# Kernel optimization log

Measured on AMD Instinct MI355X. Metric: run time of the kernel, lower is better.

The kernel has to match this reference:

```python
import jax, jax.numpy as jnp
import numpy as np

B, S, D, H = 2, 2048, 1024, 16
HD = D // H  # head_dim = 64


def setup_inputs() -> dict:
    key = jax.random.key(0)
    k1, k2, k3 = jax.random.split(key, 3)
    x = jax.random.normal(k1, (B, S, D), dtype=jnp.float32)
    mask = jnp.zeros((B, S, S), dtype=jnp.float32)  # additive mask
    # Dense(3*D) params (glorot-ish scale) and Dense(D) output projection
    Wqkv = jax.random.normal(k2, (D, 3 * D), dtype=jnp.float32) * (1.0 / np.sqrt(D))
    bqkv = jnp.zeros((3 * D,), dtype=jnp.float32)
    Wo = jax.random.normal(k3, (D, D), dtype=jnp.float32) * (1.0 / np.sqrt(D))
    bo = jnp.zeros((D,), dtype=jnp.float32)
    return {"x": x, "mask": mask, "Wqkv": Wqkv, "bqkv": bqkv, "Wo": Wo, "bo": bo}


def reference(x, mask, Wqkv, bqkv, Wo, bo):
    b, s, d = x.shape
    qkv = x @ Wqkv + bqkv                              # [B,S,3D]
    qkv = qkv.reshape(b, s, H, 3 * HD).transpose(0, 2, 1, 3)  # [B,H,S,3*HD]
    q, k, v = jnp.split(qkv, 3, axis=-1)               # each [B,H,S,HD]
    scale = 1.0 / jnp.sqrt(jnp.float32(HD))
    scores = jnp.einsum('bhqd,bhkd->bhqk', q, k) * scale  # [B,H,S,S]
    scores = scores + mask[:, None, :, :]
    attn = jax.nn.softmax(scores, axis=-1)
    values = jnp.einsum('bhqk,bhkd->bhqd', attn, v)    # [B,H,S,HD]
    # Faithful to original: reshape WITHOUT transposing heads back
    values = values.reshape(b, s, H * HD)              # [B,S,D]
    return values @ Wo + bo
```

## Files before the change

### kernel.cpp

```cpp
#include <hip/hip_runtime.h>
#include <hip/hip_bf16.h>

#define B_ 2
#define S_ 2048
#define D_ 1024
#define H_ 16
#define HD_ 64

typedef __attribute__((ext_vector_type(8))) short short8;
typedef __attribute__((ext_vector_type(4))) float f32x4;
typedef __attribute__((ext_vector_type(16))) float f32x16;
typedef __attribute__((ext_vector_type(4))) unsigned short us4;

static __device__ __forceinline__ ushort f2bf(float x) {
  __hip_bfloat16 h = __float2bfloat16(x);
  return *reinterpret_cast<ushort*>(&h);
}

static __device__ __forceinline__ void gld_lds16(void* lds, const void* g) {
  __builtin_amdgcn_global_load_lds(
      (__attribute__((address_space(1))) void*)(g),
      (__attribute__((address_space(3))) void*)(lds), 16, 0, 0);
}


static __device__ __forceinline__ void transpose_tile(const float* __restrict__ in,
                                                      ushort* __restrict__ out,
                                                      int K, int N, int bn, int bk,
                                                      int tx, int ty) {
  __shared__ float tile[32][33];
  #pragma unroll
  for (int i = ty; i < 32; i += 8)
    tile[i][tx] = in[(size_t)(bk + i) * N + bn + tx];
  __syncthreads();
  #pragma unroll
  for (int i = ty; i < 32; i += 8)
    out[(size_t)(bn + i) * K + bk + tx] = f2bf(tile[tx][i]);
}

__global__ __launch_bounds__(256) void prep_all(const float4* __restrict__ x4,
                                                ushort* __restrict__ xbf,
                                                const float* __restrict__ Wqkv,
                                                ushort* __restrict__ wqkvT,
                                                const float* __restrict__ Wo,
                                                ushort* __restrict__ woT) {
  const int blk = blockIdx.x, tid = threadIdx.x;
  if (blk < 4096) {
    const int i = blk * 256 + tid;
    float4 v = x4[i];
    ushort4 o;
    o.x = f2bf(v.x); o.y = f2bf(v.y); o.z = f2bf(v.z); o.w = f2bf(v.w);
    *reinterpret_cast<ushort4*>(xbf + (size_t)i * 4) = o;
  } else if (blk < 7168) {
    const int sub = blk - 4096;
    transpose_tile(Wqkv, wqkvT, D_, 3 * D_, (sub % 96) * 32, (sub / 96) * 32,
                   tid & 31, tid >> 5);
  } else {
    const int sub = blk - 7168;
    transpose_tile(Wo, woT, D_, D_, (sub % 32) * 32, (sub / 32) * 32,
                   tid & 31, tid >> 5);
  }
}

template <bool OUT_BF16>
__global__ __launch_bounds__(256) void gemm_bt(const ushort* __restrict__ A,
                                               const ushort* __restrict__ Bt,
                                               const float* __restrict__ bias,
                                               ushort* __restrict__ Cb,
                                               float* __restrict__ Cf,
                                               int M, int N, int K) {
  __shared__ __align__(16) ushort As[128 * 32];
  __shared__ __align__(16) ushort Bs[128 * 32];
  const int tid = threadIdx.x;
  const int lane = tid & 63, wid = tid >> 6;
  const int wr = wid >> 1, wc = wid & 1;

  const int nwg = gridDim.x * gridDim.y;
  const int lin = blockIdx.x + gridDim.x * blockIdx.y;
  const int nl = (lin & 7) * (nwg >> 3) + (lin >> 3);
  const int row0 = (nl % gridDim.x) * 128, col0 = (nl / gridDim.x) * 128;

  const int l15 = lane & 15, lhi = lane >> 4;

  f32x4 acc[4][4];
  #pragma unroll
  for (int i = 0; i < 4; ++i)
    #pragma unroll
    for (int j = 0; j < 4; ++j)
      acc[i][j] = f32x4{0.f, 0.f, 0.f, 0.f};

  const int sr = tid >> 2;
  const int scol = (tid & 3) * 8;

  for (int k0 = 0; k0 < K; k0 += 32) {
    gld_lds16(&As[(size_t)tid * 8],        &A[(size_t)(row0 + sr) * K + k0 + scol]);
    gld_lds16(&As[2048 + (size_t)tid * 8], &A[(size_t)(row0 + 64 + sr) * K + k0 + scol]);
    gld_lds16(&Bs[(size_t)tid * 8],        &Bt[(size_t)(col0 + sr) * K + k0 + scol]);
    gld_lds16(&Bs[2048 + (size_t)tid * 8], &Bt[(size_t)(col0 + 64 + sr) * K + k0 + scol]);
    __syncthreads();

    short8 af[4], bfr[4];
    #pragma unroll
    for (int mt = 0; mt < 4; ++mt)
      af[mt] = *(const short8*)&As[(wr * 64 + mt * 16 + l15) * 32 + lhi * 8];
    #pragma unroll
    for (int nt = 0; nt < 4; ++nt)
      bfr[nt] = *(const short8*)&Bs[(wc * 64 + nt * 16 + l15) * 32 + lhi * 8];
    #pragma unroll
    for (int mt = 0; mt < 4; ++mt)
      #pragma unroll
      for (int nt = 0; nt < 4; ++nt)
        acc[mt][nt] = __builtin_amdgcn_mfma_f32_16x16x32_bf16(af[mt], bfr[nt], acc[mt][nt], 0, 0, 0);
    __syncthreads();
  }

  const int orow = row0 + wr * 64;
  const int ocol = col0 + wc * 64 + l15;
  #pragma unroll
  for (int mt = 0; mt < 4; ++mt) {
    #pragma unroll
    for (int nt = 0; nt < 4; ++nt) {
      const int gc = ocol + nt * 16;
      const float bv = bias[gc];
      #pragma unroll
      for (int r = 0; r < 4; ++r) {
        const int gr = orow + mt * 16 + lhi * 4 + r;
        const float v = acc[mt][nt][r] + bv;
        if (OUT_BF16) Cb[(size_t)gr * N + gc] = f2bf(v);
        else          Cf[(size_t)gr * N + gc] = v;
      }
    }
  }
}

__global__ __launch_bounds__(256, 2) void flash_attn(const ushort* __restrict__ qkv,
                                                     const float* __restrict__ mask,
                                                     ushort* __restrict__ values) {
  __shared__ __align__(16) ushort Ks[2][64 * 64];
  __shared__ __align__(16) ushort Vt[2][64 * 64];

  const int tid = threadIdx.x;
  const int lane = tid & 63, wid = tid >> 6;
  const int l31 = lane & 31, lhalf = lane >> 5;
  const int qt = blockIdx.x, bh = blockIdx.y, b = bh >> 4, h = bh & 15;
  const size_t base = (size_t)b * S_ * 3072 + (size_t)h * 192;
  const int q = qt * 128 + wid * 32 + l31;
  const int NT = S_ / 64;

  short8 qf[4];
  {
    const ushort* qrow = qkv + base + (size_t)q * 3072 + lhalf * 8;
    qf[0] = *(const short8*)(qrow);
    qf[1] = *(const short8*)(qrow + 16);
    qf[2] = *(const short8*)(qrow + 32);
    qf[3] = *(const short8*)(qrow + 48);
  }

  const int srow = tid >> 3, sch = tid & 7;
  const int hsr = (srow ^ (srow >> 3)) & 7;
  const int scs = sch ^ hsr;
  const int kg = tid & 15, d0 = (tid >> 4) * 4;
  const int skg = (kg & 12) | ((kg & 1) << 1) | ((kg >> 1) & 1);

  float m_run = -3.0e38f, l_run = 0.f;
  f32x16 o[2];
  #pragma unroll
  for (int dg = 0; dg < 2; ++dg)
    #pragma unroll
    for (int i = 0; i < 16; ++i) o[dg][i] = 0.f;

  const float* mrow = mask + ((size_t)b * S_ + q) * S_;
  us4 vr[4];
  f32x16 scA[2], scB[2];

#define QKT_(SCDST, KSBUF)                                                     \
  {                                                                            \
    _Pragma("unroll")                                                          \
    for (int g = 0; g < 2; ++g) {                                              \
      const int row_ = g * 32 + l31;                                           \
      const int hk_ = (row_ ^ (row_ >> 3)) & 7;                                \
      const ushort* kp_ = &(KSBUF)[row_ * 64];                                 \
      f32x16 s_;                                                               \
      _Pragma("unroll")                                                        \
      for (int i = 0; i < 16; ++i) s_[i] = 0.f;                                \
      _Pragma("unroll")                                                        \
      for (int kd = 0; kd < 4; ++kd) {                                         \
        short8 kf_ = *(const short8*)&kp_[(((kd * 2 + lhalf) ^ hk_) & 7) * 8]; \
        s_ = __builtin_amdgcn_mfma_f32_32x32x16_bf16(kf_, qf[kd], s_, 0, 0, 0);\
      }                                                                        \
      (SCDST)[g] = s_;                                                         \
    }                                                                          \
  }

#define VSCATTER_(VTBUF)                                                       \
  {                                                                            \
    _Pragma("unroll")                                                          \
    for (int dd = 0; dd < 4; ++dd) {                                           \
      const int d_ = d0 + dd;                                                  \
      const int hd_ = (d_ ^ (d_ >> 3)) & 7;                                    \
      us4 w_;                                                                  \
      w_[0] = vr[0][dd]; w_[1] = vr[1][dd];                                    \
      w_[2] = vr[2][dd]; w_[3] = vr[3][dd];                                    \
      *(us4*)&(VTBUF)[d_ * 64 + (((skg >> 1) ^ hd_) & 7) * 8 + (skg & 1) * 4] = w_; \
    }                                                                          \
  }

#define HALF_(T, SCCUR, SCNEXT)                                                \
  {                                                                            \
    const int t_ = (T);                                                        \
    const bool pre1_ = (t_ + 1 < NT), pre2_ = (t_ + 2 < NT);                   \
    if (pre2_) {                                                               \
      const ushort* kn_ = qkv + base + (size_t)(t_ + 2) * 64 * 3072 +          \
                          (size_t)srow * 3072 + 64;                            \
      gld_lds16(&Ks[t_ & 1][tid * 8],        kn_ + scs * 8);                   \
      gld_lds16(&Ks[t_ & 1][2048 + tid * 8], kn_ + (size_t)32 * 3072 + (scs ^ 4) * 8); \
    }                                                                          \
    if (pre1_) {                                                               \
      const ushort* vn_ = qkv + base + (size_t)(t_ + 1) * 64 * 3072 + 128 + d0;\
      _Pragma("unroll")                                                        \
      for (int kk = 0; kk < 4; ++kk)                                           \
        vr[kk] = *(const us4*)(vn_ + (size_t)(kg * 4 + kk) * 3072);            \
    }                                                                          \
    f32x4 mk_[8];                                                              \
    {                                                                          \
      const float* mp_ = mrow + t_ * 64 + lhalf * 4;                           \
      _Pragma("unroll")                                                        \
      for (int i = 0; i < 8; ++i)                                              \
        mk_[i] = *(const f32x4*)(mp_ + (i >> 2) * 32 + (i & 3) * 8);           \
    }                                                                          \
    __builtin_amdgcn_s_setprio(1);                                             \
    if (pre1_) QKT_(SCNEXT, Ks[(t_ + 1) & 1]);                                 \
    _Pragma("unroll")                                                          \
    for (int g = 0; g < 2; ++g)                                                \
      _Pragma("unroll")                                                        \
      for (int r = 0; r < 16; ++r)                                             \
        (SCCUR)[g][r] = (SCCUR)[g][r] * 0.125f + mk_[g * 4 + (r >> 2)][r & 3]; \
    float mx_ = (SCCUR)[0][0];                                                 \
    _Pragma("unroll")                                                          \
    for (int g = 0; g < 2; ++g)                                                \
      _Pragma("unroll")                                                        \
      for (int r = 0; r < 16; ++r) mx_ = fmaxf(mx_, (SCCUR)[g][r]);            \
    mx_ = fmaxf(mx_, __shfl_xor(mx_, 32));                                     \
    if (__any(mx_ > m_run + 8.0f)) {                                           \
      const float mnew_ = fmaxf(m_run, mx_);                                   \
      const float alpha_ = __expf(m_run - mnew_);                              \
      m_run = mnew_;                                                           \
      l_run *= alpha_;                                                         \
      _Pragma("unroll")                                                        \
      for (int dg = 0; dg < 2; ++dg)                                           \
        _Pragma("unroll")                                                      \
        for (int i = 0; i < 16; ++i) o[dg][i] *= alpha_;                       \
    }                                                                          \
    float ps_ = 0.f;                                                           \
    _Pragma("unroll")                                                          \
    for (int g = 0; g < 2; ++g)                                                \
      _Pragma("unroll")                                                        \
      for (int r = 0; r < 16; ++r) {                                           \
        const float p_ = __expf((SCCUR)[g][r] - m_run);                        \
        (SCCUR)[g][r] = p_;                                                    \
        ps_ += p_;                                                             \
      }                                                                        \
    ps_ += __shfl_xor(ps_, 32);                                                \
    l_run += ps_;                                                              \
    short8 pf_[4];                                                             \
    _Pragma("unroll")                                                          \
    for (int ks = 0; ks < 4; ++ks)                                             \
      _Pragma("unroll")                                                        \
      for (int j = 0; j < 8; ++j)                                              \
        pf_[ks][j] = (short)f2bf((SCCUR)[ks >> 1][8 * (ks & 1) + j]);          \
    _Pragma("unroll")                                                          \
    for (int dg = 0; dg < 2; ++dg) {                                           \
      const int d_ = dg * 32 + l31;                                            \
      const int hv_ = (d_ ^ (d_ >> 3)) & 7;                                    \
      const ushort* vp_ = &Vt[t_ & 1][d_ * 64];                                \
      _Pragma("unroll")                                                        \
      for (int ks = 0; ks < 4; ++ks) {                                         \
        short8 vf_ = *(const short8*)&vp_[(((ks * 2 + lhalf) ^ hv_) & 7) * 8]; \
        o[dg] = __builtin_amdgcn_mfma_f32_32x32x16_bf16(vf_, pf_[ks], o[dg], 0, 0, 0); \
      }                                                                        \
    }                                                                          \
    __builtin_amdgcn_s_setprio(0);                                             \
    if (pre1_) VSCATTER_(Vt[(t_ + 1) & 1]);                                    \
    __syncthreads();                                                           \
  }

  {
    const ushort* k0 = qkv + base + (size_t)srow * 3072 + 64;
    gld_lds16(&Ks[0][tid * 8],        k0 + scs * 8);
    gld_lds16(&Ks[0][2048 + tid * 8], k0 + (size_t)32 * 3072 + (scs ^ 4) * 8);
    const ushort* k1 = k0 + (size_t)64 * 3072;
    gld_lds16(&Ks[1][tid * 8],        k1 + scs * 8);
    gld_lds16(&Ks[1][2048 + tid * 8], k1 + (size_t)32 * 3072 + (scs ^ 4) * 8);
    #pragma unroll
    for (int kk = 0; kk < 4; ++kk)
      vr[kk] = *(const us4*)(qkv + base + (size_t)(kg * 4 + kk) * 3072 + 128 + d0);
    VSCATTER_(Vt[0]);
    __syncthreads();
    QKT_(scA, Ks[0]);
  }

  for (int tp = 0; tp < NT; tp += 2) {
    HALF_(tp,     scA, scB);
    HALF_(tp + 1, scB, scA);
  }

  const float inv = 1.0f / l_run;
  ushort* vout = values + ((size_t)bh * S_ + q) * 64;
  #pragma unroll
  for (int dg = 0; dg < 2; ++dg)
    #pragma unroll
    for (int quad = 0; quad < 4; ++quad) {
      us4 w;
      #pragma unroll
      for (int r = 0; r < 4; ++r) w[r] = f2bf(o[dg][quad * 4 + r] * inv);
      *(us4*)(vout + dg * 32 + quad * 8 + lhalf * 4) = w;
    }
#undef HALF_
#undef VSCATTER_
#undef QKT_
}


extern "C" void kernel_launch(void* const* d_in, const int* in_sizes, int n_in,
                              void* d_out, int out_size, void* d_ws, size_t ws_size,
                              hipStream_t stream) {
  const float* x    = (const float*)d_in[0];
  const float* mask = (const float*)d_in[1];
  const float* Wqkv = (const float*)d_in[2];
  const float* bqkv = (const float*)d_in[3];
  const float* Wo   = (const float*)d_in[4];
  const float* bo   = (const float*)d_in[5];
  float* out = (float*)d_out;

  char* ws = (char*)d_ws;
  ushort* xbf    = (ushort*)(ws + 0);
  ushort* vals   = (ushort*)(ws + 0);
  ushort* wqkvT  = (ushort*)(ws + 8388608);
  ushort* woT    = (ushort*)(ws + 14680064);
  ushort* qkv    = (ushort*)(ws + 16777216);

  prep_all<<<8192, 256, 0, stream>>>((const float4*)x, xbf, Wqkv, wqkvT, Wo, woT);
  gemm_bt<true><<<dim3((B_ * S_) / 128, (3 * D_) / 128), 256, 0, stream>>>(
      xbf, wqkvT, bqkv, qkv, nullptr, B_ * S_, 3 * D_, D_);
  flash_attn<<<dim3(S_ / 128, B_ * H_), 256, 0, stream>>>(qkv, mask, vals);
  gemm_bt<false><<<dim3((B_ * S_) / 128, D_ / 128), 256, 0, stream>>>(
      vals, woT, bo, nullptr, out, B_ * S_, D_, D_);
}
```

Baseline: 182.0 us.

## Split KV sequence across two wave groups per block and merge softmax partials in LDS

The attention block grows from 256 to 512 threads. Two groups of four waves each process half of the key/value sequence for the same 128 queries, using separate double-buffered K/V tiles in LDS. At the end, group 1 writes its partial output, running max and running sum to LDS, and group 0 combines the two with a log-sum-exp rescale before writing bf16 values. This raises the number of waves in flight per query tile to hide latency, at the cost of doubled LDS use per block, a higher register-pressure target from the launch bounds (512, 4), and an extra merge step.

```diff
diff --git a/kernel.cpp b/kernel.cpp
--- a/kernel.cpp
+++ b/kernel.cpp
@@ -133,19 +133,21 @@
   }
 }
 
-__global__ __launch_bounds__(256, 2) void flash_attn(const ushort* __restrict__ qkv,
+__global__ __launch_bounds__(512, 4) void flash_attn(const ushort* __restrict__ qkv,
                                                      const float* __restrict__ mask,
                                                      ushort* __restrict__ values) {
-  __shared__ __align__(16) ushort Ks[2][64 * 64];
-  __shared__ __align__(16) ushort Vt[2][64 * 64];
+  __shared__ __align__(16) ushort Ks[2][2][64 * 64];
+  __shared__ __align__(16) ushort Vt[2][2][64 * 64];
 
   const int tid = threadIdx.x;
   const int lane = tid & 63, wid = tid >> 6;
+  const int grp = wid >> 2, wi = wid & 2 ? (wid & 3) : (wid & 3);
   const int l31 = lane & 31, lhalf = lane >> 5;
   const int qt = blockIdx.x, bh = blockIdx.y, b = bh >> 4, h = bh & 15;
   const size_t base = (size_t)b * S_ * 3072 + (size_t)h * 192;
-  const int q = qt * 128 + wid * 32 + l31;
-  const int NT = S_ / 64;
+  const size_t gkoff = (size_t)grp * 1024 * 3072;
+  const int q = qt * 128 + (wid & 3) * 32 + l31;
+  const int NT = 16;
 
   short8 qf[4];
   {
@@ -156,10 +158,11 @@
     qf[3] = *(const short8*)(qrow + 48);
   }
 
-  const int srow = tid >> 3, sch = tid & 7;
+  const int ltid = tid & 255;
+  const int srow = ltid >> 3, sch = ltid & 7;
   const int hsr = (srow ^ (srow >> 3)) & 7;
   const int scs = sch ^ hsr;
-  const int kg = tid & 15, d0 = (tid >> 4) * 4;
+  const int kg = ltid & 15, d0 = (ltid >> 4) * 4;
   const int skg = (kg & 12) | ((kg & 1) << 1) | ((kg >> 1) & 1);
 
   float m_run = -3.0e38f, l_run = 0.f;
@@ -169,7 +172,7 @@
     #pragma unroll
     for (int i = 0; i < 16; ++i) o[dg][i] = 0.f;
 
-  const float* mrow = mask + ((size_t)b * S_ + q) * S_;
+  const float* mrow = mask + ((size_t)b * S_ + q) * S_ + grp * 1024;
   us4 vr[4];
   f32x16 scA[2], scB[2];
 
@@ -210,13 +213,13 @@
     const int t_ = (T);                                                        \
     const bool pre1_ = (t_ + 1 < NT), pre2_ = (t_ + 2 < NT);                   \
     if (pre2_) {                                                               \
-      const ushort* kn_ = qkv + base + (size_t)(t_ + 2) * 64 * 3072 +          \
+      const ushort* kn_ = qkv + base + gkoff + (size_t)(t_ + 2) * 64 * 3072 +  \
                           (size_t)srow * 3072 + 64;                            \
-      gld_lds16(&Ks[t_ & 1][tid * 8],        kn_ + scs * 8);                   \
-      gld_lds16(&Ks[t_ & 1][2048 + tid * 8], kn_ + (size_t)32 * 3072 + (scs ^ 4) * 8); \
+      gld_lds16(&Ks[grp][t_ & 1][ltid * 8],        kn_ + scs * 8);             \
+      gld_lds16(&Ks[grp][t_ & 1][2048 + ltid * 8], kn_ + (size_t)32 * 3072 + (scs ^ 4) * 8); \
     }                                                                          \
     if (pre1_) {                                                               \
-      const ushort* vn_ = qkv + base + (size_t)(t_ + 1) * 64 * 3072 + 128 + d0;\
+      const ushort* vn_ = qkv + base + gkoff + (size_t)(t_ + 1) * 64 * 3072 + 128 + d0; \
       _Pragma("unroll")                                                        \
       for (int kk = 0; kk < 4; ++kk)                                           \
         vr[kk] = *(const us4*)(vn_ + (size_t)(kg * 4 + kk) * 3072);            \
@@ -229,7 +232,7 @@
         mk_[i] = *(const f32x4*)(mp_ + (i >> 2) * 32 + (i & 3) * 8);           \
     }                                                                          \
     __builtin_amdgcn_s_setprio(1);                                             \
-    if (pre1_) QKT_(SCNEXT, Ks[(t_ + 1) & 1]);                                 \
+    if (pre1_) QKT_(SCNEXT, Ks[grp][(t_ + 1) & 1]);                            \
     _Pragma("unroll")                                                          \
     for (int g = 0; g < 2; ++g)                                                \
       _Pragma("unroll")                                                        \
@@ -272,7 +275,7 @@
     for (int dg = 0; dg < 2; ++dg) {                                           \
       const int d_ = dg * 32 + l31;                                            \
       const int hv_ = (d_ ^ (d_ >> 3)) & 7;                                    \
-      const ushort* vp_ = &Vt[t_ & 1][d_ * 64];                                \
+      const ushort* vp_ = &Vt[grp][t_ & 1][d_ * 64];                           \
       _Pragma("unroll")                                                        \
       for (int ks = 0; ks < 4; ++ks) {                                         \
         short8 vf_ = *(const short8*)&vp_[(((ks * 2 + lhalf) ^ hv_) & 7) * 8]; \
@@ -280,23 +283,23 @@
       }                                                                        \
     }                                                                          \
     __builtin_amdgcn_s_setprio(0);                                             \
-    if (pre1_) VSCATTER_(Vt[(t_ + 1) & 1]);                                    \
+    if (pre1_) VSCATTER_(Vt[grp][(t_ + 1) & 1]);                               \
     __syncthreads();                                                           \
   }
 
   {
-    const ushort* k0 = qkv + base + (size_t)srow * 3072 + 64;
-    gld_lds16(&Ks[0][tid * 8],        k0 + scs * 8);
-    gld_lds16(&Ks[0][2048 + tid * 8], k0 + (size_t)32 * 3072 + (scs ^ 4) * 8);
+    const ushort* k0 = qkv + base + gkoff + (size_t)srow * 3072 + 64;
+    gld_lds16(&Ks[grp][0][ltid * 8],        k0 + scs * 8);
+    gld_lds16(&Ks[grp][0][2048 + ltid * 8], k0 + (size_t)32 * 3072 + (scs ^ 4) * 8);
     const ushort* k1 = k0 + (size_t)64 * 3072;
-    gld_lds16(&Ks[1][tid * 8],        k1 + scs * 8);
-    gld_lds16(&Ks[1][2048 + tid * 8], k1 + (size_t)32 * 3072 + (scs ^ 4) * 8);
+    gld_lds16(&Ks[grp][1][ltid * 8],        k1 + scs * 8);
+    gld_lds16(&Ks[grp][1][2048 + ltid * 8], k1 + (size_t)32 * 3072 + (scs ^ 4) * 8);
     #pragma unroll
     for (int kk = 0; kk < 4; ++kk)
-      vr[kk] = *(const us4*)(qkv + base + (size_t)(kg * 4 + kk) * 3072 + 128 + d0);
-    VSCATTER_(Vt[0]);
+      vr[kk] = *(const us4*)(qkv + base + gkoff + (size_t)(kg * 4 + kk) * 3072 + 128 + d0);
+    VSCATTER_(Vt[grp][0]);
     __syncthreads();
-    QKT_(scA, Ks[0]);
+    QKT_(scA, Ks[grp][0]);
   }
 
   for (int tp = 0; tp < NT; tp += 2) {
@@ -304,17 +307,41 @@
     HALF_(tp + 1, scB, scA);
   }
 
-  const float inv = 1.0f / l_run;
-  ushort* vout = values + ((size_t)bh * S_ + q) * 64;
-  #pragma unroll
-  for (int dg = 0; dg < 2; ++dg)
-    #pragma unroll
-    for (int quad = 0; quad < 4; ++quad) {
-      us4 w;
+  float* cb   = (float*)&Vt[0][0][0];
+  float2* cml = (float2*)&Ks[0][0][0];
+  const int qloc = (wid & 3) * 32 + l31;
+  const int cswz = (qloc & 7) << 3;
+  if (grp == 1) {
+    #pragma unroll
+    for (int dg = 0; dg < 2; ++dg)
       #pragma unroll
-      for (int r = 0; r < 4; ++r) w[r] = f2bf(o[dg][quad * 4 + r] * inv);
-      *(us4*)(vout + dg * 32 + quad * 8 + lhalf * 4) = w;
-    }
+      for (int quad = 0; quad < 4; ++quad) {
+        f32x4 w;
+        #pragma unroll
+        for (int r = 0; r < 4; ++r) w[r] = o[dg][quad * 4 + r];
+        *(f32x4*)&cb[qloc * 64 + ((dg * 32 + quad * 8 + lhalf * 4) ^ cswz)] = w;
+      }
+    if (lhalf == 0) cml[qloc] = make_float2(m_run, l_run);
+  }
+  __syncthreads();
+  if (grp == 0) {
+    const float2 ml1 = cml[qloc];
+    const float m = fmaxf(m_run, ml1.x);
+    const float w0 = __expf(m_run - m), w1 = __expf(ml1.x - m);
+    const float inv = 1.0f / (l_run * w0 + ml1.y * w1);
+    ushort* vout = values + ((size_t)bh * S_ + q) * 64;
+    #pragma unroll
+    for (int dg = 0; dg < 2; ++dg)
+      #pragma unroll
+      for (int quad = 0; quad < 4; ++quad) {
+        const f32x4 o1 = *(const f32x4*)&cb[qloc * 64 + ((dg * 32 + quad * 8 + lhalf * 4) ^ cswz)];
+        us4 w;
+        #pragma unroll
+        for (int r = 0; r < 4; ++r)
+          w[r] = f2bf((o[dg][quad * 4 + r] * w0 + o1[r] * w1) * inv);
+        *(us4*)(vout + dg * 32 + quad * 8 + lhalf * 4) = w;
+      }
+  }
 #undef HALF_
 #undef VSCATTER_
 #undef QKT_
@@ -342,7 +369,7 @@
   prep_all<<<8192, 256, 0, stream>>>((const float4*)x, xbf, Wqkv, wqkvT, Wo, woT);
   gemm_bt<true><<<dim3((B_ * S_) / 128, (3 * D_) / 128), 256, 0, stream>>>(
       xbf, wqkvT, bqkv, qkv, nullptr, B_ * S_, 3 * D_, D_);
-  flash_attn<<<dim3(S_ / 128, B_ * H_), 256, 0, stream>>>(qkv, mask, vals);
+  flash_attn<<<dim3(S_ / 128, B_ * H_), 512, 0, stream>>>(qkv, mask, vals);
   gemm_bt<false><<<dim3((B_ * S_) / 128, D_ / 128), 256, 0, stream>>>(
       vals, woT, bo, nullptr, out, B_ * S_, D_, D_);
 }
```

Result: slower. 475.1 us (+161.0%).
